# Kernel optimization log

Measured on AMD Instinct MI355X. Metric: run time of the kernel, lower is better.

## Reference

```python
import jax, jax.numpy as jnp
import numpy as np

H = 16  # heads


def setup_inputs() -> dict:
    key = jax.random.key(0)
    ks = jax.random.split(key, 10)
    B, S, M = 4, 2048, 1024
    scale = 1.0 / np.sqrt(M)
    return {
        "x": jax.random.normal(ks[0], (B, S, M), dtype=jnp.float32),
        "mask": jax.random.uniform(ks[1], (B, 1, S, S), dtype=jnp.float32),
        "Wq": jax.random.normal(ks[2], (M, M), dtype=jnp.float32) * scale,
        "bq": jax.random.normal(ks[3], (M,), dtype=jnp.float32) * scale,
        "Wk": jax.random.normal(ks[4], (M, M), dtype=jnp.float32) * scale,
        "bk": jax.random.normal(ks[5], (M,), dtype=jnp.float32) * scale,
        "Wv": jax.random.normal(ks[6], (M, M), dtype=jnp.float32) * scale,
        "bv": jax.random.normal(ks[7], (M,), dtype=jnp.float32) * scale,
        "Wo": jax.random.normal(ks[8], (M, M), dtype=jnp.float32) * scale,
        "bo": jax.random.normal(ks[9], (M,), dtype=jnp.float32) * scale,
    }


def reference(x, mask, Wq, bq, Wk, bk, Wv, bv, Wo, bo):
    B, S, M = x.shape
    dk = M // H
    # QKV projections (torch Linear: x @ W.T + b), then split heads -> [B,H,S,dk]
    q = (x @ Wq.T + bq).reshape(B, S, H, dk).transpose(0, 2, 1, 3)
    k = (x @ Wk.T + bk).reshape(B, S, H, dk).transpose(0, 2, 1, 3)
    v = (x @ Wv.T + bv).reshape(B, S, H, dk).transpose(0, 2, 1, 3)
    # scores: [B,H,S,S], multiplicative mask (non-standard!) then softmax
    scores = jnp.einsum("bhqd,bhkd->bhqk", q, k) / jnp.sqrt(jnp.float32(dk))
    scores = scores * mask  # mask broadcasts over heads
    attn = jax.nn.softmax(scores, axis=-1)
    # dropout is identity in eval/reference mode
    out = jnp.einsum("bhqk,bhkd->bhqd", attn, v)  # [B,H,S,dk]
    concat = out.transpose(0, 2, 1, 3).reshape(B, S, M)
    return concat @ Wo.T + bo
```

## Files before the change

kernel.cpp:

```cpp
#include <hip/hip_runtime.h>

typedef __attribute__((ext_vector_type(8))) short s16x8;
typedef __attribute__((ext_vector_type(4))) short s16x4;
typedef __attribute__((ext_vector_type(4))) float f32x4;
typedef __attribute__((ext_vector_type(2))) float f32x2;
typedef __attribute__((ext_vector_type(16))) float f32x16;
typedef __attribute__((ext_vector_type(2))) unsigned int u32x2;

#define DEV static __device__ __forceinline__

DEV void gload_lds16(const void* g, void* l) {
  __builtin_amdgcn_global_load_lds(
      (const __attribute__((address_space(1))) void*)g,
      (__attribute__((address_space(3))) void*)l, 16, 0, 0);
}

DEV unsigned short f2bf(float f) {
  unsigned int u = __float_as_uint(f);
  u = (u + 0x7fffu + ((u >> 16) & 1u)) >> 16;
  return (unsigned short)u;
}

DEV unsigned pk2(float lo, float hi) {
  unsigned r;
  asm("v_cvt_pk_bf16_f32 %0, %1, %2" : "=v"(r) : "v"(lo), "v"(hi));
  return r;
}

DEV float exp2_fast(float x) {
  float r;
  asm("v_exp_f32 %0, %1" : "=v"(r) : "v"(x));
  return r;
}

DEV f32x2 pk_mul(f32x2 a, f32x2 b) {
  f32x2 d;
  asm("v_pk_mul_f32 %0, %1, %2" : "=v"(d) : "v"(a), "v"(b));
  return d;
}

DEV f32x2 pk_add(f32x2 a, f32x2 b) {
  f32x2 d;
  asm("v_pk_add_f32 %0, %1, %2" : "=v"(d) : "v"(a), "v"(b));
  return d;
}

DEV float swap32_add(float x) {
  const u32x2 r = __builtin_amdgcn_permlane32_swap(__float_as_uint(x), __float_as_uint(x),
                                                   false, false);
  return __uint_as_float(r.x) + __uint_as_float(r.y);
}

DEV void cvt8(const float* __restrict__ in, unsigned short* __restrict__ out, int i) {
  float4 a = *(const float4*)(in + i);
  float4 b = *(const float4*)(in + i + 4);
  union { s16x8 v; unsigned short u[8]; } o;
  o.u[0] = f2bf(a.x); o.u[1] = f2bf(a.y); o.u[2] = f2bf(a.z); o.u[3] = f2bf(a.w);
  o.u[4] = f2bf(b.x); o.u[5] = f2bf(b.y); o.u[6] = f2bf(b.z); o.u[7] = f2bf(b.w);
  *(s16x8*)(out + i) = o.v;
}

__global__ __launch_bounds__(256) void k_prep(
    const float* __restrict__ x, const float* __restrict__ mask,
    const float* __restrict__ Wq, const float* __restrict__ Wk,
    const float* __restrict__ Wv, const float* __restrict__ Wo,
    unsigned short* __restrict__ xb, unsigned short* __restrict__ wcat,
    unsigned short* __restrict__ slab) {
  __shared__ unsigned short Mt[128 * 68];
  const int bid = blockIdx.x;
  const int tid = threadIdx.x;
  if (bid < 4096) {
    cvt8(x, xb, (bid * 256 + tid) * 8);
    return;
  }
  if (bid < 6144) {
    const int id = bid - 4096;
    const int sel = id >> 9;
    const float* in = (sel == 0) ? Wq : (sel == 1) ? Wk : (sel == 2) ? Wv : Wo;
    cvt8(in, wcat + sel * 1048576, ((id & 511) * 256 + tid) * 8);
    return;
  }
  const int id = bid - 6144;
  const int t = id & 31, qt = (id >> 5) & 15, b = id >> 9;
  const float* src = mask + (size_t)b * 4194304 + (size_t)qt * 128 * 2048 + t * 64;
#pragma unroll
  for (int it = 0; it < 8; ++it) {
    const int c = it * 256 + tid;
    const int row = c >> 4, kc = c & 15;
    const float4 v = *(const float4*)(src + (size_t)row * 2048 + kc * 4);
    unsigned short* d = Mt + row * 68 + kc * 4;
    d[0] = f2bf(v.x); d[1] = f2bf(v.y); d[2] = f2bf(v.z); d[3] = f2bf(v.w);
  }
  __syncthreads();
  unsigned short* dst = slab + ((((size_t)b * 16 + qt) * 32 + t) * 8192);
#pragma unroll
  for (int it = 0; it < 4; ++it) {
    const int c = it * 256 + tid;
    const int w = c >> 8, i2 = (c >> 6) & 3, ln = c & 63;
    const int qrow = w * 32 + (ln & 31);
    const int kbase = 32 * (i2 >> 1) + 16 * (i2 & 1) + 4 * (ln >> 5);
    union { s16x8 v; s16x4 h[2]; } o;
    o.h[0] = *(const s16x4*)(Mt + qrow * 68 + kbase);
    o.h[1] = *(const s16x4*)(Mt + qrow * 68 + kbase + 8);
    *(s16x8*)(dst + c * 8) = o.v;
  }
}

__global__ __launch_bounds__(256) void k_gemm_qkv(
    const unsigned short* __restrict__ A, const unsigned short* __restrict__ Bcat,
    const float* __restrict__ bq, const float* __restrict__ bk,
    const float* __restrict__ bv,
    unsigned short* __restrict__ outQK, unsigned short* __restrict__ vtw) {
  constexpr int K = 1024;
  constexpr float QSC = 0.125f * 1.44269504f;
  __shared__ unsigned short As[128 * 64];
  __shared__ unsigned short Bs[128 * 64];

  const int lin = blockIdx.x;
  const int logical = (lin & 7) * 192 + (lin >> 3);
  const int nb = logical % 24;
  const int mb = logical / 24;
  const int m0 = mb * 128;
  const int n0 = nb * 128;
  const int z = n0 >> 10;

  const int tid = threadIdx.x;
  const int lane = tid & 63;
  const int l15 = lane & 15, g = lane >> 4;
  const int w = tid >> 6;
  const int wr = w >> 1, wc = w & 1;

  const int sr = tid >> 3;
  const int sc = tid & 7;

  f32x4 acc[4][4] = {};

  for (int kt = 0; kt < K / 64; ++kt) {
#pragma unroll
    for (int i = 0; i < 4; ++i) {
      const int row = i * 32 + sr;
      gload_lds16(A + (size_t)(m0 + row) * K + kt * 64 + ((sc ^ (row & 7)) * 8),
                  (void*)(As + i * 2048 + tid * 8));
      gload_lds16(Bcat + (size_t)(n0 + row) * K + kt * 64 + ((sc ^ (row & 7)) * 8),
                  (void*)(Bs + i * 2048 + tid * 8));
    }
    __syncthreads();
#pragma unroll
    for (int ks = 0; ks < 2; ++ks) {
      s16x8 af[4], bf[4];
#pragma unroll
      for (int i = 0; i < 4; ++i) {
        const int ra = wr * 64 + i * 16 + l15;
        af[i] = *(const s16x8*)(As + ra * 64 + (((ks * 4 + g) ^ (ra & 7)) * 8));
        const int rb = wc * 64 + i * 16 + l15;
        bf[i] = *(const s16x8*)(Bs + rb * 64 + (((ks * 4 + g) ^ (rb & 7)) * 8));
      }
#pragma unroll
      for (int i = 0; i < 4; ++i)
#pragma unroll
        for (int j = 0; j < 4; ++j)
          acc[i][j] = __builtin_amdgcn_mfma_f32_16x16x32_bf16(af[i], bf[j], acc[i][j], 0, 0, 0);
    }
    __syncthreads();
  }

  const float* bias = (z == 0) ? bq : (z == 1) ? bk : bv;
  const float osc = (z == 0) ? QSC : 1.0f;
#pragma unroll
  for (int j = 0; j < 4; ++j) {
    const int gcol = n0 + wc * 64 + j * 16 + l15;
    const int col = gcol & 1023;
    const float bvv = bias[col];
    const int h = col >> 6, d = col & 63;
#pragma unroll
    for (int i = 0; i < 4; ++i) {
      const int grow0 = m0 + wr * 64 + i * 16 + g * 4;
      const int bb = grow0 >> 11, s0 = grow0 & 2047;
      if (z < 2) {
        unsigned short* outp = outQK + (size_t)z * 8388608;
#pragma unroll
        for (int r = 0; r < 4; ++r)
          outp[(((size_t)(bb * 16 + h) * 2048 + (s0 + r)) << 6) + d] =
              f2bf((acc[i][j][r] + bvv) * osc);
      } else {
        union { s16x4 v; unsigned short u[4]; } pk;
#pragma unroll
        for (int r = 0; r < 4; ++r) pk.u[r] = f2bf(acc[i][j][r] + bvv);
        *(s16x4*)(vtw + (((size_t)(bb * 16 + h)) << 17) + (size_t)d * 2048 + s0) = pk.v;
      }
    }
  }
}

__global__ __launch_bounds__(256) void k_gemm_o(
    const unsigned short* __restrict__ A, const unsigned short* __restrict__ Bw,
    const float* __restrict__ bias, float* __restrict__ outp) {
  constexpr int K = 1024;
  __shared__ unsigned short As[128 * 64];
  __shared__ unsigned short Bs[64 * 64];

  const int lin = blockIdx.x;
  const int logical = (lin & 7) * 128 + (lin >> 3);
  const int nb = logical & 15;
  const int mb = logical >> 4;
  const int m0 = mb * 128, n0 = nb * 64;

  const int tid = threadIdx.x;
  const int lane = tid & 63;
  const int l15 = lane & 15, g = lane >> 4;
  const int w = tid >> 6;
  const int wr = w >> 1, wc = w & 1;

  const int sr = tid >> 3;
  const int sc = tid & 7;

  f32x4 acc[4][2] = {};

  for (int kt = 0; kt < K / 64; ++kt) {
#pragma unroll
    for (int i = 0; i < 4; ++i) {
      const int row = i * 32 + sr;
      gload_lds16(A + (size_t)(m0 + row) * K + kt * 64 + ((sc ^ (row & 7)) * 8),
                  (void*)(As + i * 2048 + tid * 8));
    }
#pragma unroll
    for (int i = 0; i < 2; ++i) {
      const int row = i * 32 + sr;
      gload_lds16(Bw + (size_t)(n0 + row) * K + kt * 64 + ((sc ^ (row & 7)) * 8),
                  (void*)(Bs + i * 2048 + tid * 8));
    }
    __syncthreads();
#pragma unroll
    for (int ks = 0; ks < 2; ++ks) {
      s16x8 af[4], bf[2];
#pragma unroll
      for (int mi = 0; mi < 4; ++mi) {
        const int ra = wr * 64 + mi * 16 + l15;
        af[mi] = *(const s16x8*)(As + ra * 64 + (((ks * 4 + g) ^ (ra & 7)) * 8));
      }
#pragma unroll
      for (int nj = 0; nj < 2; ++nj) {
        const int rb = wc * 32 + nj * 16 + l15;
        bf[nj] = *(const s16x8*)(Bs + rb * 64 + (((ks * 4 + g) ^ (rb & 7)) * 8));
      }
#pragma unroll
      for (int mi = 0; mi < 4; ++mi)
#pragma unroll
        for (int nj = 0; nj < 2; ++nj)
          acc[mi][nj] =
              __builtin_amdgcn_mfma_f32_16x16x32_bf16(af[mi], bf[nj], acc[mi][nj], 0, 0, 0);
    }
    __syncthreads();
  }

#pragma unroll
  for (int nj = 0; nj < 2; ++nj) {
    const int gcol = n0 + wc * 32 + nj * 16 + l15;
    const float bv = bias[gcol];
#pragma unroll
    for (int mi = 0; mi < 4; ++mi)
#pragma unroll
      for (int r = 0; r < 4; ++r) {
        const int grow = m0 + wr * 64 + mi * 16 + g * 4 + r;
        outp[(size_t)grow * 1024 + gcol] = acc[mi][nj][r] + bv;
      }
  }
}

__global__ __launch_bounds__(512) void k_attn9(
    const unsigned short* __restrict__ q, const unsigned short* __restrict__ k,
    const unsigned short* __restrict__ vt, const unsigned short* __restrict__ slab,
    unsigned short* __restrict__ concat) {
  __shared__ unsigned short Ks[2][64 * 64];
  __shared__ unsigned short Vs[2][64 * 64];

  const int tid = threadIdx.x;
  const int lane = tid & 63;
  const int w = tid >> 6;
  const int ww = w & 3;
  const int l31 = lane & 31;
  const int hh = lane >> 5;

  const int lin = blockIdx.x + 16 * (blockIdx.y + 8 * blockIdx.z);
  const int logical = (lin & 7) * 64 + (lin >> 3);
  const int h = logical & 15;
  const int qtb = (logical >> 4) & 7;
  const int b = logical >> 7;
  const int qt128 = qtb * 2 + (w >> 2);

  const size_t bhO = (size_t)(b * 16 + h) * (2048 * 64);
  const unsigned short* kb = k + bhO;
  const unsigned short* vb = vt + bhO;
  const int qg = qt128 * 128 + ww * 32 + l31;

  s16x8 qf[4];
  {
    const unsigned short* qp = q + bhO + (size_t)qg * 64 + hh * 8;
#pragma unroll
    for (int kd = 0; kd < 4; ++kd) qf[kd] = *(const s16x8*)(qp + kd * 16);
  }

  const unsigned short* mp =
      slab + ((((size_t)b * 16 + qt128) * 32) * 8192) + ((size_t)(ww * 4) * 64 + lane) * 8;

  float l_r = 0.f;
  f32x16 oacc[2] = {};

  const int srow = tid >> 3;
  const int sc = tid & 7;

#define STAGE(BUF, T_)                                                                \
  {                                                                                   \
    const int kv0s = (T_)*64;                                                         \
    const int sz = (sc ^ (srow & 7)) * 8;                                             \
    gload_lds16(kb + (size_t)(kv0s + srow) * 64 + sz, (void*)(Ks[BUF] + tid * 8));    \
    gload_lds16(vb + (size_t)srow * 2048 + kv0s + sz, (void*)(Vs[BUF] + tid * 8));    \
  }

  STAGE(0, 0)
  __syncthreads();

  for (int tt = 0; tt < 16; ++tt) {
#pragma unroll
    for (int half = 0; half < 2; ++half) {
      const int t = tt * 2 + half;

      s16x8 mv[4];
#pragma unroll
      for (int i2 = 0; i2 < 4; ++i2) mv[i2] = *(const s16x8*)(mp + i2 * 512);
      mp += 8192;

      if (t < 31) STAGE(half ^ 1, t + 1)

      f32x16 sacc[2] = {};
      __builtin_amdgcn_s_setprio(1);
#pragma unroll
      for (int f = 0; f < 2; ++f) {
        const int rk = f * 32 + l31;
        const unsigned short* Kr = Ks[half] + rk * 64;
        const int swb = rk & 7;
#pragma unroll
        for (int kd = 0; kd < 4; ++kd) {
          const s16x8 kf = *(const s16x8*)(Kr + (((kd * 2 + hh) ^ swb) * 8));
          sacc[f] = __builtin_amdgcn_mfma_f32_32x32x16_bf16(kf, qf[kd], sacc[f], 0, 0, 0);
        }
      }
      __builtin_amdgcn_s_setprio(0);

      f32x2 u[16];
#pragma unroll
      for (int f = 0; f < 2; ++f)
#pragma unroll
        for (int kk = 0; kk < 2; ++kk) {
          union { s16x8 v; unsigned d[4]; } mw;
          mw.v = mv[f * 2 + kk];
#pragma unroll
          for (int d = 0; d < 4; ++d) {
            const unsigned m = mw.d[d];
            f32x2 mpv, sp;
            mpv.x = __uint_as_float(m << 16);
            mpv.y = __uint_as_float(m & 0xffff0000u);
            sp.x = sacc[f][kk * 8 + d * 2];
            sp.y = sacc[f][kk * 8 + d * 2 + 1];
            u[f * 8 + kk * 4 + d] = pk_mul(sp, mpv);
          }
        }
#pragma unroll
      for (int j = 0; j < 16; ++j) {
        u[j].x = exp2_fast(u[j].x);
        u[j].y = exp2_fast(u[j].y);
      }

      {
        f32x2 t8[8];
#pragma unroll
        for (int j = 0; j < 8; ++j) t8[j] = pk_add(u[2 * j], u[2 * j + 1]);
        f32x2 t4[4];
#pragma unroll
        for (int j = 0; j < 4; ++j) t4[j] = pk_add(t8[2 * j], t8[2 * j + 1]);
        const f32x2 t2a = pk_add(t4[0], t4[1]);
        const f32x2 t2b = pk_add(t4[2], t4[3]);
        const f32x2 t1 = pk_add(t2a, t2b);
        l_r += swap32_add(t1.x + t1.y);
      }

#pragma unroll
      for (int ks = 0; ks < 4; ++ks) {
        const unsigned X0 = pk2(u[ks * 4 + 0].x, u[ks * 4 + 0].y);
        const unsigned X1 = pk2(u[ks * 4 + 1].x, u[ks * 4 + 1].y);
        const unsigned Y0 = pk2(u[ks * 4 + 2].x, u[ks * 4 + 2].y);
        const unsigned Y1 = pk2(u[ks * 4 + 3].x, u[ks * 4 + 3].y);
        const u32x2 r0 = __builtin_amdgcn_permlane32_swap(X0, Y0, false, false);
        const u32x2 r1 = __builtin_amdgcn_permlane32_swap(X1, Y1, false, false);
        union { s16x8 v; unsigned u[4]; } pf;
        pf.u[0] = r0.x; pf.u[1] = r1.x; pf.u[2] = r0.y; pf.u[3] = r1.y;
        __builtin_amdgcn_s_setprio(1);
#pragma unroll
        for (int df = 0; df < 2; ++df) {
          const int rv = df * 32 + l31;
          const s16x8 vf =
              *(const s16x8*)(Vs[half] + rv * 64 + (((ks * 2 + hh) ^ (rv & 7)) * 8));
          oacc[df] = __builtin_amdgcn_mfma_f32_32x32x16_bf16(vf, pf.v, oacc[df], 0, 0, 0);
        }
        __builtin_amdgcn_s_setprio(0);
      }
      __syncthreads();
    }
  }
#undef STAGE

  const float inv = 1.0f / l_r;
  unsigned short* cb = concat + ((size_t)b * 2048 + qg) * 1024 + h * 64;
#pragma unroll
  for (int df = 0; df < 2; ++df)
#pragma unroll
    for (int r = 0; r < 16; r += 2) {
      const int d = df * 32 + (r & 3) + 8 * (r >> 2) + 4 * hh;
      const unsigned uo = (unsigned)f2bf(oacc[df][r] * inv) |
                          ((unsigned)f2bf(oacc[df][r + 1] * inv) << 16);
      *(unsigned*)(cb + d) = uo;
    }
}

extern "C" void kernel_launch(void* const* d_in, const int* in_sizes, int n_in,
                              void* d_out, int out_size, void* d_ws, size_t ws_size,
                              hipStream_t stream) {
  const float* x    = (const float*)d_in[0];
  const float* mask = (const float*)d_in[1];
  const float* Wq   = (const float*)d_in[2];
  const float* bq   = (const float*)d_in[3];
  const float* Wk   = (const float*)d_in[4];
  const float* bk   = (const float*)d_in[5];
  const float* Wv   = (const float*)d_in[6];
  const float* bv   = (const float*)d_in[7];
  const float* Wo   = (const float*)d_in[8];
  const float* bo   = (const float*)d_in[9];

  char* ws = (char*)d_ws;
  unsigned short* xb    = (unsigned short*)(ws);
  unsigned short* wcat  = (unsigned short*)(ws + (size_t)16777216);
  unsigned short* wob   = wcat + 3 * 1048576;
  unsigned short* qw    = (unsigned short*)(ws + (size_t)25165824);
  unsigned short* kw    = qw + 8388608;
  unsigned short* vtw   = (unsigned short*)(ws + (size_t)58720256);
  unsigned short* slab  = (unsigned short*)(ws + (size_t)75497472);
  unsigned short* cw    = xb;

  k_prep<<<dim3(8192), dim3(256), 0, stream>>>(x, mask, Wq, Wk, Wv, Wo, xb, wcat, slab);
  k_gemm_qkv<<<dim3(1536), dim3(256), 0, stream>>>(xb, wcat, bq, bk, bv, qw, vtw);
  k_attn9<<<dim3(16, 8, 4), dim3(512), 0, stream>>>(qw, kw, vtw, slab, cw);
  k_gemm_o<<<dim3(1024), dim3(256), 0, stream>>>(cw, wob, bo, (float*)d_out);
}
```

Before: 232.1 us.

## Software-pipeline attention loop: overlap PV of previous tile with QK and softmax

Restructures the attention inner loop so the P·V matrix multiply for tile t-1 runs while tile t's QK^T and softmax are computed, keeping packed probabilities in registers across iterations. V staging grows to four LDS buffers so the previous tile's V stays valid while new tiles load. The per-iteration cross-half lane reduction of the row sum is moved to a single reduction after the loop. The aim is to hide the exp/pack latency behind MFMA work, at the cost of more registers and LDS, which can lower occupancy.

```diff
diff --git a/kernel.cpp b/kernel.cpp
--- a/kernel.cpp
+++ b/kernel.cpp
@@ -267,12 +267,12 @@
   }
 }
 
-__global__ __launch_bounds__(512) void k_attn9(
+__global__ __launch_bounds__(512) void k_attn10(
     const unsigned short* __restrict__ q, const unsigned short* __restrict__ k,
     const unsigned short* __restrict__ vt, const unsigned short* __restrict__ slab,
     unsigned short* __restrict__ concat) {
   __shared__ unsigned short Ks[2][64 * 64];
-  __shared__ unsigned short Vs[2][64 * 64];
+  __shared__ unsigned short Vs[4][64 * 64];
 
   const int tid = threadIdx.x;
   const int lane = tid & 63;
@@ -300,116 +300,136 @@
     for (int kd = 0; kd < 4; ++kd) qf[kd] = *(const s16x8*)(qp + kd * 16);
   }
 
-  const unsigned short* mp =
+  const unsigned short* mp0 =
       slab + ((((size_t)b * 16 + qt128) * 32) * 8192) + ((size_t)(ww * 4) * 64 + lane) * 8;
 
   float l_r = 0.f;
   f32x16 oacc[2] = {};
+  s16x8 pf_prev[4];
 
   const int srow = tid >> 3;
   const int sc = tid & 7;
-
-#define STAGE(BUF, T_)                                                                \
+  const int ssz = (sc ^ (srow & 7)) * 8;
+
+#define STAGE(T_)                                                                     \
   {                                                                                   \
     const int kv0s = (T_)*64;                                                         \
-    const int sz = (sc ^ (srow & 7)) * 8;                                             \
-    gload_lds16(kb + (size_t)(kv0s + srow) * 64 + sz, (void*)(Ks[BUF] + tid * 8));    \
-    gload_lds16(vb + (size_t)srow * 2048 + kv0s + sz, (void*)(Vs[BUF] + tid * 8));    \
-  }
-
-  STAGE(0, 0)
+    gload_lds16(kb + (size_t)(kv0s + srow) * 64 + ssz,                                \
+                (void*)(Ks[(T_)&1] + tid * 8));                                       \
+    gload_lds16(vb + (size_t)srow * 2048 + kv0s + ssz,                                \
+                (void*)(Vs[(T_)&3] + tid * 8));                                       \
+  }
+
+#define SOFTMAX_PACK(PFN)                                                             \
+  {                                                                                   \
+    f32x2 u[16];                                                                      \
+    _Pragma("unroll") for (int f = 0; f < 2; ++f)                                     \
+      _Pragma("unroll") for (int kk = 0; kk < 2; ++kk) {                              \
+        union { s16x8 v; unsigned d[4]; } mw;                                         \
+        mw.v = mv[f * 2 + kk];                                                        \
+        _Pragma("unroll") for (int d = 0; d < 4; ++d) {                               \
+          const unsigned m = mw.d[d];                                                 \
+          f32x2 mpv, sp;                                                              \
+          mpv.x = __uint_as_float(m << 16);                                           \
+          mpv.y = __uint_as_float(m & 0xffff0000u);                                   \
+          sp.x = sacc[f][kk * 8 + d * 2];                                             \
+          sp.y = sacc[f][kk * 8 + d * 2 + 1];                                         \
+          u[f * 8 + kk * 4 + d] = pk_mul(sp, mpv);                                    \
+        }                                                                             \
+      }                                                                               \
+    _Pragma("unroll") for (int j = 0; j < 16; ++j) {                                  \
+      u[j].x = exp2_fast(u[j].x);                                                     \
+      u[j].y = exp2_fast(u[j].y);                                                     \
+    }                                                                                 \
+    f32x2 t8[8];                                                                      \
+    _Pragma("unroll") for (int j = 0; j < 8; ++j) t8[j] = pk_add(u[2 * j], u[2 * j + 1]); \
+    f32x2 t4[4];                                                                      \
+    _Pragma("unroll") for (int j = 0; j < 4; ++j) t4[j] = pk_add(t8[2 * j], t8[2 * j + 1]); \
+    const f32x2 t2a = pk_add(t4[0], t4[1]);                                           \
+    const f32x2 t2b = pk_add(t4[2], t4[3]);                                           \
+    const f32x2 t1 = pk_add(t2a, t2b);                                                \
+    l_r += t1.x + t1.y;                                                               \
+    _Pragma("unroll") for (int ks = 0; ks < 4; ++ks) {                                \
+      const unsigned X0 = pk2(u[ks * 4 + 0].x, u[ks * 4 + 0].y);                      \
+      const unsigned X1 = pk2(u[ks * 4 + 1].x, u[ks * 4 + 1].y);                      \
+      const unsigned Y0 = pk2(u[ks * 4 + 2].x, u[ks * 4 + 2].y);                      \
+      const unsigned Y1 = pk2(u[ks * 4 + 3].x, u[ks * 4 + 3].y);                      \
+      const u32x2 r0 = __builtin_amdgcn_permlane32_swap(X0, Y0, false, false);        \
+      const u32x2 r1 = __builtin_amdgcn_permlane32_swap(X1, Y1, false, false);        \
+      union { s16x8 v; unsigned u4[4]; } pfu;                                         \
+      pfu.u4[0] = r0.x; pfu.u4[1] = r1.x; pfu.u4[2] = r0.y; pfu.u4[3] = r1.y;         \
+      PFN[ks] = pfu.v;                                                                \
+    }                                                                                 \
+  }
+
+#define QKT(T_)                                                                       \
+  f32x16 sacc[2] = {};                                                                \
+  {                                                                                   \
+    const unsigned short* Kbuf = Ks[(T_)&1];                                          \
+    __builtin_amdgcn_s_setprio(1);                                                    \
+    _Pragma("unroll") for (int f = 0; f < 2; ++f) {                                   \
+      const int rk = f * 32 + l31;                                                    \
+      const unsigned short* Kr = Kbuf + rk * 64;                                      \
+      const int swb = rk & 7;                                                         \
+      _Pragma("unroll") for (int kd = 0; kd < 4; ++kd) {                              \
+        const s16x8 kf = *(const s16x8*)(Kr + (((kd * 2 + hh) ^ swb) * 8));           \
+        sacc[f] = __builtin_amdgcn_mfma_f32_32x32x16_bf16(kf, qf[kd], sacc[f], 0, 0, 0); \
+      }                                                                               \
+    }                                                                                 \
+    __builtin_amdgcn_s_setprio(0);                                                    \
+  }
+
+#define PV_PREV(T_)                                                                   \
+  {                                                                                   \
+    const unsigned short* Vbuf = Vs[(T_)&3];                                          \
+    __builtin_amdgcn_s_setprio(1);                                                    \
+    _Pragma("unroll") for (int ks = 0; ks < 4; ++ks)                                  \
+      _Pragma("unroll") for (int df = 0; df < 2; ++df) {                              \
+        const int rv = df * 32 + l31;                                                 \
+        const s16x8 vf =                                                              \
+            *(const s16x8*)(Vbuf + rv * 64 + (((ks * 2 + hh) ^ (rv & 7)) * 8));       \
+        oacc[df] = __builtin_amdgcn_mfma_f32_32x32x16_bf16(vf, pf_prev[ks], oacc[df], 0, 0, 0); \
+      }                                                                               \
+    __builtin_amdgcn_s_setprio(0);                                                    \
+  }
+
+  STAGE(0)
   __syncthreads();
-
-  for (int tt = 0; tt < 16; ++tt) {
-#pragma unroll
-    for (int half = 0; half < 2; ++half) {
-      const int t = tt * 2 + half;
-
-      s16x8 mv[4];
-#pragma unroll
-      for (int i2 = 0; i2 < 4; ++i2) mv[i2] = *(const s16x8*)(mp + i2 * 512);
-      mp += 8192;
-
-      if (t < 31) STAGE(half ^ 1, t + 1)
-
-      f32x16 sacc[2] = {};
-      __builtin_amdgcn_s_setprio(1);
-#pragma unroll
-      for (int f = 0; f < 2; ++f) {
-        const int rk = f * 32 + l31;
-        const unsigned short* Kr = Ks[half] + rk * 64;
-        const int swb = rk & 7;
-#pragma unroll
-        for (int kd = 0; kd < 4; ++kd) {
-          const s16x8 kf = *(const s16x8*)(Kr + (((kd * 2 + hh) ^ swb) * 8));
-          sacc[f] = __builtin_amdgcn_mfma_f32_32x32x16_bf16(kf, qf[kd], sacc[f], 0, 0, 0);
-        }
-      }
-      __builtin_amdgcn_s_setprio(0);
-
-      f32x2 u[16];
-#pragma unroll
-      for (int f = 0; f < 2; ++f)
-#pragma unroll
-        for (int kk = 0; kk < 2; ++kk) {
-          union { s16x8 v; unsigned d[4]; } mw;
-          mw.v = mv[f * 2 + kk];
-#pragma unroll
-          for (int d = 0; d < 4; ++d) {
-            const unsigned m = mw.d[d];
-            f32x2 mpv, sp;
-            mpv.x = __uint_as_float(m << 16);
-            mpv.y = __uint_as_float(m & 0xffff0000u);
-            sp.x = sacc[f][kk * 8 + d * 2];
-            sp.y = sacc[f][kk * 8 + d * 2 + 1];
-            u[f * 8 + kk * 4 + d] = pk_mul(sp, mpv);
-          }
-        }
-#pragma unroll
-      for (int j = 0; j < 16; ++j) {
-        u[j].x = exp2_fast(u[j].x);
-        u[j].y = exp2_fast(u[j].y);
-      }
-
-      {
-        f32x2 t8[8];
-#pragma unroll
-        for (int j = 0; j < 8; ++j) t8[j] = pk_add(u[2 * j], u[2 * j + 1]);
-        f32x2 t4[4];
-#pragma unroll
-        for (int j = 0; j < 4; ++j) t4[j] = pk_add(t8[2 * j], t8[2 * j + 1]);
-        const f32x2 t2a = pk_add(t4[0], t4[1]);
-        const f32x2 t2b = pk_add(t4[2], t4[3]);
-        const f32x2 t1 = pk_add(t2a, t2b);
-        l_r += swap32_add(t1.x + t1.y);
-      }
-
-#pragma unroll
-      for (int ks = 0; ks < 4; ++ks) {
-        const unsigned X0 = pk2(u[ks * 4 + 0].x, u[ks * 4 + 0].y);
-        const unsigned X1 = pk2(u[ks * 4 + 1].x, u[ks * 4 + 1].y);
-        const unsigned Y0 = pk2(u[ks * 4 + 2].x, u[ks * 4 + 2].y);
-        const unsigned Y1 = pk2(u[ks * 4 + 3].x, u[ks * 4 + 3].y);
-        const u32x2 r0 = __builtin_amdgcn_permlane32_swap(X0, Y0, false, false);
-        const u32x2 r1 = __builtin_amdgcn_permlane32_swap(X1, Y1, false, false);
-        union { s16x8 v; unsigned u[4]; } pf;
-        pf.u[0] = r0.x; pf.u[1] = r1.x; pf.u[2] = r0.y; pf.u[3] = r1.y;
-        __builtin_amdgcn_s_setprio(1);
-#pragma unroll
-        for (int df = 0; df < 2; ++df) {
-          const int rv = df * 32 + l31;
-          const s16x8 vf =
-              *(const s16x8*)(Vs[half] + rv * 64 + (((ks * 2 + hh) ^ (rv & 7)) * 8));
-          oacc[df] = __builtin_amdgcn_mfma_f32_32x32x16_bf16(vf, pf.v, oacc[df], 0, 0, 0);
-        }
-        __builtin_amdgcn_s_setprio(0);
-      }
-      __syncthreads();
-    }
-  }
+  {
+    s16x8 mv[4];
+#pragma unroll
+    for (int i2 = 0; i2 < 4; ++i2) mv[i2] = *(const s16x8*)(mp0 + i2 * 512);
+    STAGE(1)
+    QKT(0)
+    SOFTMAX_PACK(pf_prev)
+    __syncthreads();
+  }
+
+  for (int t = 1; t < 32; ++t) {
+    s16x8 mv[4];
+    const unsigned short* mpt = mp0 + (size_t)t * 8192;
+#pragma unroll
+    for (int i2 = 0; i2 < 4; ++i2) mv[i2] = *(const s16x8*)(mpt + i2 * 512);
+
+    if (t < 31) STAGE(t + 1)
+
+    QKT(t)
+    PV_PREV(t - 1)
+    s16x8 pfn[4];
+    SOFTMAX_PACK(pfn)
+#pragma unroll
+    for (int ks = 0; ks < 4; ++ks) pf_prev[ks] = pfn[ks];
+    __syncthreads();
+  }
+
+  PV_PREV(31)
+
 #undef STAGE
-
-  const float inv = 1.0f / l_r;
+#undef SOFTMAX_PACK
+#undef QKT
+#undef PV_PREV
+
+  const float inv = 1.0f / swap32_add(l_r);
   unsigned short* cb = concat + ((size_t)b * 2048 + qg) * 1024 + h * 64;
 #pragma unroll
   for (int df = 0; df < 2; ++df)
@@ -448,6 +468,6 @@
 
   k_prep<<<dim3(8192), dim3(256), 0, stream>>>(x, mask, Wq, Wk, Wv, Wo, xb, wcat, slab);
   k_gemm_qkv<<<dim3(1536), dim3(256), 0, stream>>>(xb, wcat, bq, bk, bv, qw, vtw);
-  k_attn9<<<dim3(16, 8, 4), dim3(512), 0, stream>>>(qw, kw, vtw, slab, cw);
+  k_attn10<<<dim3(16, 8, 4), dim3(512), 0, stream>>>(qw, kw, vtw, slab, cw);
   k_gemm_o<<<dim3(1024), dim3(256), 0, stream>>>(cw, wob, bo, (float*)d_out);
 }
```

Result: slower. 237.3 us (+2.2%).

## Split attention head dimension across waves to cut registers and double block count

Applied to the files above, without the earlier changes.

Each block now covers one 128-query tile instead of two. Its two wave groups split the 64-wide output head dimension into halves, and each wave keeps a single 32x32 output accumulator and one score tile at a time. The grid doubles and the launch bounds request higher occupancy. The aim is lower register pressure and better latency hiding. The cost is that QK^T, mask loads and exp are computed twice per query row, and K/V are staged into LDS by twice as many blocks.

```diff
diff --git a/kernel.cpp b/kernel.cpp
--- a/kernel.cpp
+++ b/kernel.cpp
@@ -267,7 +267,7 @@
   }
 }
 
-__global__ __launch_bounds__(512) void k_attn9(
+__global__ __launch_bounds__(512, 8) void k_attn12(
     const unsigned short* __restrict__ q, const unsigned short* __restrict__ k,
     const unsigned short* __restrict__ vt, const unsigned short* __restrict__ slab,
     unsigned short* __restrict__ concat) {
@@ -277,21 +277,21 @@
   const int tid = threadIdx.x;
   const int lane = tid & 63;
   const int w = tid >> 6;
-  const int ww = w & 3;
+  const int qw = w & 3;
+  const int dh = w >> 2;
   const int l31 = lane & 31;
   const int hh = lane >> 5;
 
-  const int lin = blockIdx.x + 16 * (blockIdx.y + 8 * blockIdx.z);
-  const int logical = (lin & 7) * 64 + (lin >> 3);
+  const int lin = blockIdx.x + 16 * (blockIdx.y + 16 * blockIdx.z);
+  const int logical = (lin & 7) * 128 + (lin >> 3);
   const int h = logical & 15;
-  const int qtb = (logical >> 4) & 7;
-  const int b = logical >> 7;
-  const int qt128 = qtb * 2 + (w >> 2);
+  const int qt = (logical >> 4) & 15;
+  const int b = logical >> 8;
 
   const size_t bhO = (size_t)(b * 16 + h) * (2048 * 64);
   const unsigned short* kb = k + bhO;
   const unsigned short* vb = vt + bhO;
-  const int qg = qt128 * 128 + ww * 32 + l31;
+  const int qg = qt * 128 + qw * 32 + l31;
 
   s16x8 qf[4];
   {
@@ -300,126 +300,118 @@
     for (int kd = 0; kd < 4; ++kd) qf[kd] = *(const s16x8*)(qp + kd * 16);
   }
 
-  const unsigned short* mp =
-      slab + ((((size_t)b * 16 + qt128) * 32) * 8192) + ((size_t)(ww * 4) * 64 + lane) * 8;
+  const unsigned short* mp0 =
+      slab + ((((size_t)b * 16 + qt) * 32) * 8192) + ((size_t)(qw * 4) * 64 + lane) * 8;
 
   float l_r = 0.f;
-  f32x16 oacc[2] = {};
+  f32x16 oacc = {};
 
   const int srow = tid >> 3;
   const int sc = tid & 7;
-
-#define STAGE(BUF, T_)                                                                \
+  const int ssz = (sc ^ (srow & 7)) * 8;
+
+#define STAGE(T_)                                                                     \
   {                                                                                   \
     const int kv0s = (T_)*64;                                                         \
-    const int sz = (sc ^ (srow & 7)) * 8;                                             \
-    gload_lds16(kb + (size_t)(kv0s + srow) * 64 + sz, (void*)(Ks[BUF] + tid * 8));    \
-    gload_lds16(vb + (size_t)srow * 2048 + kv0s + sz, (void*)(Vs[BUF] + tid * 8));    \
-  }
-
-  STAGE(0, 0)
+    gload_lds16(kb + (size_t)(kv0s + srow) * 64 + ssz,                                \
+                (void*)(Ks[(T_)&1] + tid * 8));                                       \
+    gload_lds16(vb + (size_t)srow * 2048 + kv0s + ssz,                                \
+                (void*)(Vs[(T_)&1] + tid * 8));                                       \
+  }
+
+  STAGE(0)
   __syncthreads();
 
-  for (int tt = 0; tt < 16; ++tt) {
-#pragma unroll
-    for (int half = 0; half < 2; ++half) {
-      const int t = tt * 2 + half;
-
-      s16x8 mv[4];
-#pragma unroll
-      for (int i2 = 0; i2 < 4; ++i2) mv[i2] = *(const s16x8*)(mp + i2 * 512);
-      mp += 8192;
-
-      if (t < 31) STAGE(half ^ 1, t + 1)
-
-      f32x16 sacc[2] = {};
-      __builtin_amdgcn_s_setprio(1);
-#pragma unroll
-      for (int f = 0; f < 2; ++f) {
-        const int rk = f * 32 + l31;
-        const unsigned short* Kr = Ks[half] + rk * 64;
+  for (int t = 0; t < 32; ++t) {
+    const int cur = t & 1;
+    if (t < 31) STAGE(t + 1)
+
+    const unsigned short* mpt = mp0 + (size_t)t * 8192;
+
+#pragma unroll
+    for (int s = 0; s < 2; ++s) {
+      s16x8 mv[2];
+      mv[0] = *(const s16x8*)(mpt + (s * 2 + 0) * 512);
+      mv[1] = *(const s16x8*)(mpt + (s * 2 + 1) * 512);
+
+      f32x16 sacc = {};
+      {
+        const int rk = s * 32 + l31;
+        const unsigned short* Kr = Ks[cur] + rk * 64;
         const int swb = rk & 7;
+        __builtin_amdgcn_s_setprio(1);
 #pragma unroll
         for (int kd = 0; kd < 4; ++kd) {
           const s16x8 kf = *(const s16x8*)(Kr + (((kd * 2 + hh) ^ swb) * 8));
-          sacc[f] = __builtin_amdgcn_mfma_f32_32x32x16_bf16(kf, qf[kd], sacc[f], 0, 0, 0);
+          sacc = __builtin_amdgcn_mfma_f32_32x32x16_bf16(kf, qf[kd], sacc, 0, 0, 0);
         }
-      }
-      __builtin_amdgcn_s_setprio(0);
-
-      f32x2 u[16];
-#pragma unroll
-      for (int f = 0; f < 2; ++f)
-#pragma unroll
-        for (int kk = 0; kk < 2; ++kk) {
-          union { s16x8 v; unsigned d[4]; } mw;
-          mw.v = mv[f * 2 + kk];
-#pragma unroll
-          for (int d = 0; d < 4; ++d) {
-            const unsigned m = mw.d[d];
-            f32x2 mpv, sp;
-            mpv.x = __uint_as_float(m << 16);
-            mpv.y = __uint_as_float(m & 0xffff0000u);
-            sp.x = sacc[f][kk * 8 + d * 2];
-            sp.y = sacc[f][kk * 8 + d * 2 + 1];
-            u[f * 8 + kk * 4 + d] = pk_mul(sp, mpv);
-          }
+        __builtin_amdgcn_s_setprio(0);
+      }
+
+      f32x2 u[8];
+#pragma unroll
+      for (int kk = 0; kk < 2; ++kk) {
+        union { s16x8 v; unsigned d[4]; } mw;
+        mw.v = mv[kk];
+#pragma unroll
+        for (int d = 0; d < 4; ++d) {
+          const unsigned m = mw.d[d];
+          f32x2 mpv, sp;
+          mpv.x = __uint_as_float(m << 16);
+          mpv.y = __uint_as_float(m & 0xffff0000u);
+          sp.x = sacc[kk * 8 + d * 2];
+          sp.y = sacc[kk * 8 + d * 2 + 1];
+          u[kk * 4 + d] = pk_mul(sp, mpv);
         }
-#pragma unroll
-      for (int j = 0; j < 16; ++j) {
+      }
+#pragma unroll
+      for (int j = 0; j < 8; ++j) {
         u[j].x = exp2_fast(u[j].x);
         u[j].y = exp2_fast(u[j].y);
       }
 
       {
-        f32x2 t8[8];
-#pragma unroll
-        for (int j = 0; j < 8; ++j) t8[j] = pk_add(u[2 * j], u[2 * j + 1]);
         f32x2 t4[4];
 #pragma unroll
-        for (int j = 0; j < 4; ++j) t4[j] = pk_add(t8[2 * j], t8[2 * j + 1]);
+        for (int j = 0; j < 4; ++j) t4[j] = pk_add(u[2 * j], u[2 * j + 1]);
         const f32x2 t2a = pk_add(t4[0], t4[1]);
         const f32x2 t2b = pk_add(t4[2], t4[3]);
         const f32x2 t1 = pk_add(t2a, t2b);
-        l_r += swap32_add(t1.x + t1.y);
-      }
-
-#pragma unroll
-      for (int ks = 0; ks < 4; ++ks) {
+        l_r += t1.x + t1.y;
+      }
+
+#pragma unroll
+      for (int ks = 0; ks < 2; ++ks) {
         const unsigned X0 = pk2(u[ks * 4 + 0].x, u[ks * 4 + 0].y);
         const unsigned X1 = pk2(u[ks * 4 + 1].x, u[ks * 4 + 1].y);
         const unsigned Y0 = pk2(u[ks * 4 + 2].x, u[ks * 4 + 2].y);
         const unsigned Y1 = pk2(u[ks * 4 + 3].x, u[ks * 4 + 3].y);
         const u32x2 r0 = __builtin_amdgcn_permlane32_swap(X0, Y0, false, false);
         const u32x2 r1 = __builtin_amdgcn_permlane32_swap(X1, Y1, false, false);
-        union { s16x8 v; unsigned u[4]; } pf;
-        pf.u[0] = r0.x; pf.u[1] = r1.x; pf.u[2] = r0.y; pf.u[3] = r1.y;
+        union { s16x8 v; unsigned u4[4]; } pf;
+        pf.u4[0] = r0.x; pf.u4[1] = r1.x; pf.u4[2] = r0.y; pf.u4[3] = r1.y;
+        const int rv = dh * 32 + l31;
+        const s16x8 vf = *(const s16x8*)(
+            Vs[cur] + rv * 64 + ((((s * 4 + ks * 2 + hh)) ^ (rv & 7)) * 8));
         __builtin_amdgcn_s_setprio(1);
-#pragma unroll
-        for (int df = 0; df < 2; ++df) {
-          const int rv = df * 32 + l31;
-          const s16x8 vf =
-              *(const s16x8*)(Vs[half] + rv * 64 + (((ks * 2 + hh) ^ (rv & 7)) * 8));
-          oacc[df] = __builtin_amdgcn_mfma_f32_32x32x16_bf16(vf, pf.v, oacc[df], 0, 0, 0);
-        }
+        oacc = __builtin_amdgcn_mfma_f32_32x32x16_bf16(vf, pf.v, oacc, 0, 0, 0);
         __builtin_amdgcn_s_setprio(0);
       }
-      __syncthreads();
-    }
+    }
+
+    __syncthreads();
   }
 #undef STAGE
 
-  const float inv = 1.0f / l_r;
-  unsigned short* cb = concat + ((size_t)b * 2048 + qg) * 1024 + h * 64;
-#pragma unroll
-  for (int df = 0; df < 2; ++df)
-#pragma unroll
-    for (int r = 0; r < 16; r += 2) {
-      const int d = df * 32 + (r & 3) + 8 * (r >> 2) + 4 * hh;
-      const unsigned uo = (unsigned)f2bf(oacc[df][r] * inv) |
-                          ((unsigned)f2bf(oacc[df][r + 1] * inv) << 16);
-      *(unsigned*)(cb + d) = uo;
-    }
+  const float inv = 1.0f / swap32_add(l_r);
+  unsigned short* cb = concat + ((size_t)b * 2048 + qg) * 1024 + h * 64 + dh * 32;
+#pragma unroll
+  for (int r = 0; r < 16; r += 2) {
+    const int d = (r & 3) + 8 * (r >> 2) + 4 * hh;
+    const unsigned uo = (unsigned)f2bf(oacc[r] * inv) |
+                        ((unsigned)f2bf(oacc[r + 1] * inv) << 16);
+    *(unsigned*)(cb + d) = uo;
+  }
 }
 
 extern "C" void kernel_launch(void* const* d_in, const int* in_sizes, int n_in,
@@ -448,6 +440,6 @@
 
   k_prep<<<dim3(8192), dim3(256), 0, stream>>>(x, mask, Wq, Wk, Wv, Wo, xb, wcat, slab);
   k_gemm_qkv<<<dim3(1536), dim3(256), 0, stream>>>(xb, wcat, bq, bk, bv, qw, vtw);
-  k_attn9<<<dim3(16, 8, 4), dim3(512), 0, stream>>>(qw, kw, vtw, slab, cw);
+  k_attn12<<<dim3(16, 16, 4), dim3(512), 0, stream>>>(qw, kw, vtw, slab, cw);
   k_gemm_o<<<dim3(1024), dim3(256), 0, stream>>>(cw, wob, bo, (float*)d_out);
 }
```

After: 503.3 us. +116.8%, slower.
